# Optimization experiments

Hardware: AMD Instinct MI355X
Metric: run time of the kernel (lower is better)

## Reference

```python
import jax, jax.numpy as jnp
import numpy as np

NUM_GRAPHS = 256


def gcn_conv(x, W, b, src, dst, n_nodes):
    """PyG GCNConv: add self-loops, symmetric normalization, linear transform."""
    h = x @ W  # [N, out]
    loop = jnp.arange(n_nodes, dtype=src.dtype)
    src_f = jnp.concatenate([src, loop])  # messages j -> i, with self-loops
    dst_f = jnp.concatenate([dst, loop])
    deg = jax.ops.segment_sum(jnp.ones_like(src_f, dtype=h.dtype), dst_f,
                              num_segments=n_nodes)  # in-degree incl. self-loop
    dinv = jnp.where(deg > 0, jax.lax.rsqrt(deg), 0.0)
    norm = dinv[src_f] * dinv[dst_f]  # [E+N]
    msg = h[src_f] * norm[:, None]  # gather + scale, [E+N, out]
    out = jax.ops.segment_sum(msg, dst_f, num_segments=n_nodes)  # scatter-add
    return out + b


def global_mean_pool(x, batch, num_graphs):
    sums = jax.ops.segment_sum(x, batch, num_segments=num_graphs)
    cnt = jax.ops.segment_sum(jnp.ones((x.shape[0],), x.dtype), batch,
                              num_segments=num_graphs)
    return sums / jnp.maximum(cnt, 1.0)[:, None]


def setup_inputs() -> dict:
    key = jax.random.key(0)
    k = jax.random.split(key, 6)
    N, E, D = 50000, 800000, 133
    x = jax.random.normal(k[0], (N, D), dtype=jnp.float32)
    edge_index = jax.random.randint(k[1], (2, E), 0, N, dtype=jnp.int64)
    batch = jnp.sort(jax.random.randint(k[2], (N,), 0, NUM_GRAPHS, dtype=jnp.int64))
    s = 1.0 / np.sqrt(D)
    W1 = jax.random.normal(k[3], (D, D), dtype=jnp.float32) * s
    b1 = jnp.zeros((D,), jnp.float32)
    W2 = jax.random.normal(k[4], (D, D), dtype=jnp.float32) * s
    b2 = jnp.zeros((D,), jnp.float32)
    return {"x": x, "edge_index": edge_index, "batch": batch,
            "W1": W1, "b1": b1, "W2": W2, "b2": b2}


def reference(x, edge_index, batch, W1, b1, W2, b2):
    n = x.shape[0]
    src, dst = edge_index[0], edge_index[1]
    h = jax.nn.relu(gcn_conv(x, W1, b1, src, dst, n))
    h = jax.nn.relu(gcn_conv(h, W2, b2, src, dst, n))
    return global_mean_pool(h, batch, NUM_GRAPHS)  # [num_graphs, 133]
```

## Files before the change

kernel.cpp:

```cpp
#include <hip/hip_runtime.h>

#define D 133
#define DPB 160
#define NCGB 17
#define NGRAPH 256
#define KS 168
#define NT 9
#define CAP 64

typedef short short8 __attribute__((ext_vector_type(8)));
typedef float float4v __attribute__((ext_vector_type(4)));

__device__ __forceinline__ unsigned short f2bf(float x) {
    unsigned int u = __float_as_uint(x);
    u += 0x7fffu + ((u >> 16) & 1u);
    return (unsigned short)(u >> 16);
}

__device__ __forceinline__ void cvt8(uint4 v, float* f) {
    f[0] = __uint_as_float(v.x << 16);
    f[1] = __uint_as_float(v.x & 0xffff0000u);
    f[2] = __uint_as_float(v.y << 16);
    f[3] = __uint_as_float(v.y & 0xffff0000u);
    f[4] = __uint_as_float(v.z << 16);
    f[5] = __uint_as_float(v.z & 0xffff0000u);
    f[6] = __uint_as_float(v.w << 16);
    f[7] = __uint_as_float(v.w & 0xffff0000u);
}

__global__ __launch_bounds__(256) void k_wt(const float* __restrict__ W1,
                                            unsigned short* __restrict__ WT1,
                                            const float* __restrict__ W2,
                                            unsigned short* __restrict__ WT2,
                                            int wtB) {
    int bid = blockIdx.x;
    const float* W = (bid < wtB) ? W1 : W2;
    unsigned short* WT = (bid < wtB) ? WT1 : WT2;
    int lb = (bid < wtB) ? bid : bid - wtB;
    int i = lb * 256 + threadIdx.x;
    if (i < 144 * KS) {
        int n = i / KS, k = i - n * KS;
        WT[i] = (n < D && k < D) ? f2bf(W[(size_t)k * D + n]) : (unsigned short)0;
    }
}

__global__ __launch_bounds__(256, 2) void k_big(const float* __restrict__ X,
                                                const unsigned short* __restrict__ WTg,
                                                unsigned short* __restrict__ Y,
                                                const int* __restrict__ src,
                                                const int* __restrict__ dst,
                                                int* __restrict__ cnt,
                                                unsigned short* __restrict__ earr,
                                                const int* __restrict__ batch,
                                                int* __restrict__ gstart,
                                                int N, int E, int mt, int nib) {
    int bid = blockIdx.x, t = threadIdx.x;
    if (bid < nib) {
        int g = bid / 5, pos = bid - g * 5;
        if (pos != 4) {
            int i = (g * 4 + pos) * 256 + t;
            if (i < E) {
                int s = src[i];
                int dnode = dst[i];
                int slot = atomicAdd(&cnt[dnode], 1);
                if (slot < CAP) earr[(size_t)dnode * CAP + slot] = (unsigned short)s;
            }
            return;
        }
        int wave = t >> 6, lane = t & 63;
        int ln16 = lane & 15, quad = lane >> 4;
        int tile = g * 4 + wave;
        if (tile >= mt) return;
        int row0 = tile * 16;
        int ra = row0 + ln16; if (ra > N - 1) ra = N - 1;
        const float* Xr = X + (size_t)ra * D;
        const unsigned short* Wr = WTg + (size_t)ln16 * KS + quad * 8;

        float4v acc[NT];
        #pragma unroll
        for (int n = 0; n < NT; ++n) acc[n] = {0.f, 0.f, 0.f, 0.f};

        #pragma unroll
        for (int kk = 0; kk < 5; ++kk) {
            int cbase = kk * 32 + quad * 8;
            short8 a;
            if (kk < 4) {
                #pragma unroll
                for (int j = 0; j < 8; ++j) a[j] = (short)f2bf(Xr[cbase + j]);
            } else {
                #pragma unroll
                for (int j = 0; j < 8; ++j) {
                    int c = cbase + j;
                    a[j] = (short)((c < D) ? f2bf(Xr[c]) : 0);
                }
            }
            #pragma unroll
            for (int n = 0; n < NT; ++n) {
                short8 b = *(const short8*)(Wr + n * 16 * KS + kk * 32);
                acc[n] = __builtin_amdgcn_mfma_f32_16x16x32_bf16(a, b, acc[n], 0, 0, 0);
            }
        }
        #pragma unroll
        for (int r = 0; r < 4; ++r) {
            int row = row0 + quad * 4 + r;
            if (row < N) {
                unsigned short* Yr = Y + (size_t)row * DPB + ln16;
                #pragma unroll
                for (int n = 0; n < NT; ++n) Yr[n * 16] = f2bf(acc[n][r]);
            }
        }
        return;
    }
    bid -= nib;
    {
        int g = bid * 256 + t;
        if (g > NGRAPH) return;
        int lo = 0, hi = N;
        while (lo < hi) {
            int mid = (lo + hi) >> 1;
            if (batch[mid] < g) lo = mid + 1; else hi = mid;
        }
        gstart[g] = lo;
    }
}

__global__ __launch_bounds__(256, 2) void k_mm2(const unsigned short* __restrict__ A,
                                                const unsigned short* __restrict__ WTg,
                                                unsigned short* __restrict__ Y,
                                                int N, int mt) {
    int t = threadIdx.x;
    int wave = t >> 6, lane = t & 63;
    int ln16 = lane & 15, quad = lane >> 4;
    int tile = blockIdx.x * 4 + wave;
    if (tile >= mt) return;
    int row0 = tile * 16;
    int ra = row0 + ln16; if (ra > N - 1) ra = N - 1;
    const unsigned short* Ar = A + (size_t)ra * DPB + quad * 8;
    const unsigned short* Wr = WTg + (size_t)ln16 * KS + quad * 8;

    float4v acc[NT];
    #pragma unroll
    for (int n = 0; n < NT; ++n) acc[n] = {0.f, 0.f, 0.f, 0.f};

    #pragma unroll
    for (int kk = 0; kk < 5; ++kk) {
        short8 a = *(const short8*)(Ar + kk * 32);
        #pragma unroll
        for (int n = 0; n < NT; ++n) {
            short8 b = *(const short8*)(Wr + n * 16 * KS + kk * 32);
            acc[n] = __builtin_amdgcn_mfma_f32_16x16x32_bf16(a, b, acc[n], 0, 0, 0);
        }
    }
    #pragma unroll
    for (int r = 0; r < 4; ++r) {
        int row = row0 + quad * 4 + r;
        if (row < N) {
            unsigned short* Yr = Y + (size_t)row * DPB + ln16;
            #pragma unroll
            for (int n = 0; n < NT; ++n) Yr[n * 16] = f2bf(acc[n][r]);
        }
    }
}

__global__ __launch_bounds__(256) void k_agg(const unsigned short* __restrict__ H,
                                             const float* __restrict__ bias,
                                             const int* __restrict__ cnt,
                                             const unsigned short* __restrict__ earr,
                                             unsigned short* __restrict__ outb, int N) {
    int idx = blockIdx.x * 256 + threadIdx.x;
    if (idx >= N * NCGB) return;
    int node = idx / NCGB;
    int cg = idx - node * NCGB;
    int c = cg << 3;
    int degraw = cnt[node];
    float di = rsqrtf((float)(degraw + 1));
    float acc[8], f[8];
    uint4 hv = *(const uint4*)(H + (size_t)node * DPB + c);
    cvt8(hv, f);
    #pragma unroll
    for (int j = 0; j < 8; ++j) acc[j] = di * f[j];
    int deg = degraw > CAP ? CAP : degraw;
    const unsigned short* ep = earr + (size_t)node * CAP;
    int e = 0;
    for (; e + 4 <= deg; e += 4) {
        int s0 = ep[e], s1 = ep[e+1], s2 = ep[e+2], s3 = ep[e+3];
        float w0 = rsqrtf((float)(cnt[s0] + 1));
        float w1 = rsqrtf((float)(cnt[s1] + 1));
        float w2 = rsqrtf((float)(cnt[s2] + 1));
        float w3 = rsqrtf((float)(cnt[s3] + 1));
        uint4 v0 = *(const uint4*)(H + (size_t)s0 * DPB + c);
        uint4 v1 = *(const uint4*)(H + (size_t)s1 * DPB + c);
        uint4 v2 = *(const uint4*)(H + (size_t)s2 * DPB + c);
        uint4 v3 = *(const uint4*)(H + (size_t)s3 * DPB + c);
        cvt8(v0, f);
        #pragma unroll
        for (int j = 0; j < 8; ++j) acc[j] = fmaf(w0, f[j], acc[j]);
        cvt8(v1, f);
        #pragma unroll
        for (int j = 0; j < 8; ++j) acc[j] = fmaf(w1, f[j], acc[j]);
        cvt8(v2, f);
        #pragma unroll
        for (int j = 0; j < 8; ++j) acc[j] = fmaf(w2, f[j], acc[j]);
        cvt8(v3, f);
        #pragma unroll
        for (int j = 0; j < 8; ++j) acc[j] = fmaf(w3, f[j], acc[j]);
    }
    for (; e < deg; ++e) {
        int s = ep[e];
        float wv = rsqrtf((float)(cnt[s] + 1));
        uint4 v = *(const uint4*)(H + (size_t)s * DPB + c);
        cvt8(v, f);
        #pragma unroll
        for (int j = 0; j < 8; ++j) acc[j] = fmaf(wv, f[j], acc[j]);
    }
    float b[8];
    #pragma unroll
    for (int j = 0; j < 8; ++j) b[j] = (c + j < D) ? bias[c + j] : 0.f;
    unsigned int p[4];
    #pragma unroll
    for (int j = 0; j < 4; ++j) {
        float lo = fmaxf(fmaf(di, acc[2*j],   b[2*j]),   0.f);
        float hi = fmaxf(fmaf(di, acc[2*j+1], b[2*j+1]), 0.f);
        p[j] = (unsigned int)f2bf(lo) | ((unsigned int)f2bf(hi) << 16);
    }
    uint4 pk = {p[0], p[1], p[2], p[3]};
    unsigned short* o = outb + (size_t)node * DPB + c;
    *(uint4*)o = pk;
    if (cg == 16) {
        uint4 z = {0u, 0u, 0u, 0u};
        *(uint4*)(o + 8)  = z;
        *(uint4*)(o + 16) = z;
        *(uint4*)(o + 24) = z;
    }
}

__global__ __launch_bounds__(256) void k_pool(const unsigned short* __restrict__ H,
                                              const int* __restrict__ gstart,
                                              float* __restrict__ out) {
    int g = blockIdx.x / NCGB;
    int cg = blockIdx.x - g * NCGB;
    int c = cg << 3;
    int t = threadIdx.x;
    int s = gstart[g], e = gstart[g + 1];
    float acc[8], f[8];
    #pragma unroll
    for (int j = 0; j < 8; ++j) acc[j] = 0.f;
    for (int i = s + t; i < e; i += 256) {
        uint4 v = *(const uint4*)(H + (size_t)i * DPB + c);
        cvt8(v, f);
        #pragma unroll
        for (int j = 0; j < 8; ++j) acc[j] += f[j];
    }
    #pragma unroll
    for (int off = 32; off >= 1; off >>= 1) {
        #pragma unroll
        for (int j = 0; j < 8; ++j) acc[j] += __shfl_down(acc[j], off, 64);
    }
    __shared__ float part[4][8];
    int wave = t >> 6, lane = t & 63;
    if (lane == 0) {
        #pragma unroll
        for (int j = 0; j < 8; ++j) part[wave][j] = acc[j];
    }
    __syncthreads();
    if (t < 8) {
        int col = c + t;
        if (col < D) {
            float v = part[0][t] + part[1][t] + part[2][t] + part[3][t];
            float n = (float)(e - s);
            out[(size_t)g * D + col] = v / fmaxf(n, 1.f);
        }
    }
}

extern "C" void kernel_launch(void* const* d_in, const int* in_sizes, int n_in,
                              void* d_out, int out_size, void* d_ws, size_t ws_size,
                              hipStream_t stream) {
    const float* x   = (const float*)d_in[0];
    const int* ei    = (const int*)d_in[1];
    const int* batch = (const int*)d_in[2];
    const float* W1  = (const float*)d_in[3];
    const float* b1  = (const float*)d_in[4];
    const float* W2  = (const float*)d_in[5];
    const float* b2  = (const float*)d_in[6];
    float* out = (float*)d_out;

    int N = in_sizes[0] / D;
    int E = in_sizes[1] / 2;
    const int* src = ei;
    const int* dst = ei + E;

    char* w = (char*)d_ws;
    unsigned short* HbA = (unsigned short*)w; w += (size_t)N * DPB * 2;
    unsigned short* HbB = (unsigned short*)w; w += (size_t)N * DPB * 2;
    int* cnt            = (int*)w;            w += (size_t)N * 4;
    unsigned short* earr= (unsigned short*)w; w += (size_t)N * CAP * 2;
    int* gstart         = (int*)w;            w += (size_t)(NGRAPH + 1) * 4;
    unsigned short* WT1 = (unsigned short*)w; w += (size_t)144 * KS * 2;
    unsigned short* WT2 = (unsigned short*)w; w += (size_t)144 * KS * 2;

    int wtB   = (144 * KS + 255) / 256;
    int gsB   = (NGRAPH + 1 + 255) / 256;

    int mt = (N + 15) / 16;
    int mmB = (mt + 3) / 4;
    int nib = 5 * mmB;
    int grid_agg = (N * NCGB + 255) / 256;

    hipMemsetAsync(cnt, 0, (size_t)N * 4, stream);
    k_wt  <<<2 * wtB, 256, 0, stream>>>(W1, WT1, W2, WT2, wtB);
    k_big <<<nib + gsB, 256, 0, stream>>>(x, WT1, HbA, src, dst, cnt, earr,
                                          batch, gstart, N, E, mt, nib);
    k_agg <<<grid_agg, 256, 0, stream>>>(HbA, b1, cnt, earr, HbB, N);
    k_mm2 <<<mmB, 256, 0, stream>>>(HbB, WT2, HbA, N, mt);
    k_agg <<<grid_agg, 256, 0, stream>>>(HbA, b2, cnt, earr, HbB, N);
    k_pool<<<NGRAPH * NCGB, 256, 0, stream>>>(HbB, gstart, out);
}
```

Baseline: 257.2 us.

## Fuse layer-1 aggregation with layer-2 GEMM and fold memset into prep kernel

```diff
diff --git a/kernel.cpp b/kernel.cpp
--- a/kernel.cpp
+++ b/kernel.cpp
@@ -5,6 +5,7 @@
 #define NCGB 17
 #define NGRAPH 256
 #define KS 168
+#define LSTR 168
 #define NT 9
 #define CAP 64
 
@@ -32,15 +33,38 @@
                                             unsigned short* __restrict__ WT1,
                                             const float* __restrict__ W2,
                                             unsigned short* __restrict__ WT2,
-                                            int wtB) {
-    int bid = blockIdx.x;
-    const float* W = (bid < wtB) ? W1 : W2;
-    unsigned short* WT = (bid < wtB) ? WT1 : WT2;
-    int lb = (bid < wtB) ? bid : bid - wtB;
-    int i = lb * 256 + threadIdx.x;
-    if (i < 144 * KS) {
-        int n = i / KS, k = i - n * KS;
-        WT[i] = (n < D && k < D) ? f2bf(W[(size_t)k * D + n]) : (unsigned short)0;
+                                            int* __restrict__ cnt,
+                                            const int* __restrict__ batch,
+                                            int* __restrict__ gstart,
+                                            int N, int wtB, int czB) {
+    int bid = blockIdx.x, t = threadIdx.x;
+    if (bid < 2 * wtB) {
+        const float* W = (bid < wtB) ? W1 : W2;
+        unsigned short* WT = (bid < wtB) ? WT1 : WT2;
+        int lb = (bid < wtB) ? bid : bid - wtB;
+        int i = lb * 256 + t;
+        if (i < 144 * KS) {
+            int n = i / KS, k = i - n * KS;
+            WT[i] = (n < D && k < D) ? f2bf(W[(size_t)k * D + n]) : (unsigned short)0;
+        }
+        return;
+    }
+    bid -= 2 * wtB;
+    if (bid < czB) {
+        int i = bid * 256 + t;
+        if (i < N) cnt[i] = 0;
+        return;
+    }
+    bid -= czB;
+    {
+        int g = bid * 256 + t;
+        if (g > NGRAPH) return;
+        int lo = 0, hi = N;
+        while (lo < hi) {
+            int mid = (lo + hi) >> 1;
+            if (batch[mid] < g) lo = mid + 1; else hi = mid;
+        }
+        gstart[g] = lo;
     }
 }
 
@@ -51,91 +75,26 @@
                                                 const int* __restrict__ dst,
                                                 int* __restrict__ cnt,
                                                 unsigned short* __restrict__ earr,
-                                                const int* __restrict__ batch,
-                                                int* __restrict__ gstart,
-                                                int N, int E, int mt, int nib) {
+                                                int N, int E, int mt) {
     int bid = blockIdx.x, t = threadIdx.x;
-    if (bid < nib) {
-        int g = bid / 5, pos = bid - g * 5;
-        if (pos != 4) {
-            int i = (g * 4 + pos) * 256 + t;
-            if (i < E) {
-                int s = src[i];
-                int dnode = dst[i];
-                int slot = atomicAdd(&cnt[dnode], 1);
-                if (slot < CAP) earr[(size_t)dnode * CAP + slot] = (unsigned short)s;
-            }
-            return;
-        }
-        int wave = t >> 6, lane = t & 63;
-        int ln16 = lane & 15, quad = lane >> 4;
-        int tile = g * 4 + wave;
-        if (tile >= mt) return;
-        int row0 = tile * 16;
-        int ra = row0 + ln16; if (ra > N - 1) ra = N - 1;
-        const float* Xr = X + (size_t)ra * D;
-        const unsigned short* Wr = WTg + (size_t)ln16 * KS + quad * 8;
-
-        float4v acc[NT];
-        #pragma unroll
-        for (int n = 0; n < NT; ++n) acc[n] = {0.f, 0.f, 0.f, 0.f};
-
-        #pragma unroll
-        for (int kk = 0; kk < 5; ++kk) {
-            int cbase = kk * 32 + quad * 8;
-            short8 a;
-            if (kk < 4) {
-                #pragma unroll
-                for (int j = 0; j < 8; ++j) a[j] = (short)f2bf(Xr[cbase + j]);
-            } else {
-                #pragma unroll
-                for (int j = 0; j < 8; ++j) {
-                    int c = cbase + j;
-                    a[j] = (short)((c < D) ? f2bf(Xr[c]) : 0);
-                }
-            }
-            #pragma unroll
-            for (int n = 0; n < NT; ++n) {
-                short8 b = *(const short8*)(Wr + n * 16 * KS + kk * 32);
-                acc[n] = __builtin_amdgcn_mfma_f32_16x16x32_bf16(a, b, acc[n], 0, 0, 0);
-            }
-        }
-        #pragma unroll
-        for (int r = 0; r < 4; ++r) {
-            int row = row0 + quad * 4 + r;
-            if (row < N) {
-                unsigned short* Yr = Y + (size_t)row * DPB + ln16;
-                #pragma unroll
-                for (int n = 0; n < NT; ++n) Yr[n * 16] = f2bf(acc[n][r]);
-            }
+    int g = bid / 5, pos = bid - g * 5;
+    if (pos != 4) {
+        int i = (g * 4 + pos) * 256 + t;
+        if (i < E) {
+            int s = src[i];
+            int dnode = dst[i];
+            int slot = atomicAdd(&cnt[dnode], 1);
+            if (slot < CAP) earr[(size_t)dnode * CAP + slot] = (unsigned short)s;
         }
         return;
     }
-    bid -= nib;
-    {
-        int g = bid * 256 + t;
-        if (g > NGRAPH) return;
-        int lo = 0, hi = N;
-        while (lo < hi) {
-            int mid = (lo + hi) >> 1;
-            if (batch[mid] < g) lo = mid + 1; else hi = mid;
-        }
-        gstart[g] = lo;
-    }
-}
-
-__global__ __launch_bounds__(256, 2) void k_mm2(const unsigned short* __restrict__ A,
-                                                const unsigned short* __restrict__ WTg,
-                                                unsigned short* __restrict__ Y,
-                                                int N, int mt) {
-    int t = threadIdx.x;
     int wave = t >> 6, lane = t & 63;
     int ln16 = lane & 15, quad = lane >> 4;
-    int tile = blockIdx.x * 4 + wave;
+    int tile = g * 4 + wave;
     if (tile >= mt) return;
     int row0 = tile * 16;
     int ra = row0 + ln16; if (ra > N - 1) ra = N - 1;
-    const unsigned short* Ar = A + (size_t)ra * DPB + quad * 8;
+    const float* Xr = X + (size_t)ra * D;
     const unsigned short* Wr = WTg + (size_t)ln16 * KS + quad * 8;
 
     float4v acc[NT];
@@ -144,7 +103,18 @@
 
     #pragma unroll
     for (int kk = 0; kk < 5; ++kk) {
-        short8 a = *(const short8*)(Ar + kk * 32);
+        int cbase = kk * 32 + quad * 8;
+        short8 a;
+        if (kk < 4) {
+            #pragma unroll
+            for (int j = 0; j < 8; ++j) a[j] = (short)f2bf(Xr[cbase + j]);
+        } else {
+            #pragma unroll
+            for (int j = 0; j < 8; ++j) {
+                int c = cbase + j;
+                a[j] = (short)((c < D) ? f2bf(Xr[c]) : 0);
+            }
+        }
         #pragma unroll
         for (int n = 0; n < NT; ++n) {
             short8 b = *(const short8*)(Wr + n * 16 * KS + kk * 32);
@@ -162,11 +132,107 @@
     }
 }
 
-__global__ __launch_bounds__(256) void k_agg(const unsigned short* __restrict__ H,
-                                             const float* __restrict__ bias,
-                                             const int* __restrict__ cnt,
-                                             const unsigned short* __restrict__ earr,
-                                             unsigned short* __restrict__ outb, int N) {
+__global__ __launch_bounds__(320, 2) void k_aggmm(const unsigned short* __restrict__ H,
+                                                  const float* __restrict__ bias,
+                                                  const int* __restrict__ cnt,
+                                                  const unsigned short* __restrict__ earr,
+                                                  const unsigned short* __restrict__ WTg,
+                                                  unsigned short* __restrict__ Y, int N) {
+    __shared__ unsigned short T[16 * LSTR];
+    int t = threadIdx.x;
+    int row0 = blockIdx.x * 16;
+    if (t < 272) {
+        int l = t / NCGB;
+        int cg = t - l * NCGB;
+        int node = row0 + l;
+        if (node >= N) node = N - 1;
+        int c = cg << 3;
+        int degraw = cnt[node];
+        float di = rsqrtf((float)(degraw + 1));
+        float acc[8], f[8];
+        uint4 hv = *(const uint4*)(H + (size_t)node * DPB + c);
+        cvt8(hv, f);
+        #pragma unroll
+        for (int j = 0; j < 8; ++j) acc[j] = di * f[j];
+        int deg = degraw > CAP ? CAP : degraw;
+        const unsigned short* ep = earr + (size_t)node * CAP;
+        int e = 0;
+        for (; e + 4 <= deg; e += 4) {
+            int s0 = ep[e], s1 = ep[e+1], s2 = ep[e+2], s3 = ep[e+3];
+            float w0 = rsqrtf((float)(cnt[s0] + 1));
+            float w1 = rsqrtf((float)(cnt[s1] + 1));
+            float w2 = rsqrtf((float)(cnt[s2] + 1));
+            float w3 = rsqrtf((float)(cnt[s3] + 1));
+            uint4 v0 = *(const uint4*)(H + (size_t)s0 * DPB + c);
+            uint4 v1 = *(const uint4*)(H + (size_t)s1 * DPB + c);
+            uint4 v2 = *(const uint4*)(H + (size_t)s2 * DPB + c);
+            uint4 v3 = *(const uint4*)(H + (size_t)s3 * DPB + c);
+            cvt8(v0, f);
+            #pragma unroll
+            for (int j = 0; j < 8; ++j) acc[j] = fmaf(w0, f[j], acc[j]);
+            cvt8(v1, f);
+            #pragma unroll
+            for (int j = 0; j < 8; ++j) acc[j] = fmaf(w1, f[j], acc[j]);
+            cvt8(v2, f);
+            #pragma unroll
+            for (int j = 0; j < 8; ++j) acc[j] = fmaf(w2, f[j], acc[j]);
+            cvt8(v3, f);
+            #pragma unroll
+            for (int j = 0; j < 8; ++j) acc[j] = fmaf(w3, f[j], acc[j]);
+        }
+        for (; e < deg; ++e) {
+            int s = ep[e];
+            float wv = rsqrtf((float)(cnt[s] + 1));
+            uint4 v = *(const uint4*)(H + (size_t)s * DPB + c);
+            cvt8(v, f);
+            #pragma unroll
+            for (int j = 0; j < 8; ++j) acc[j] = fmaf(wv, f[j], acc[j]);
+        }
+        float b[8];
+        #pragma unroll
+        for (int j = 0; j < 8; ++j) b[j] = (c + j < D) ? bias[c + j] : 0.f;
+        unsigned int p[4];
+        #pragma unroll
+        for (int j = 0; j < 4; ++j) {
+            float lo = fmaxf(fmaf(di, acc[2*j],   b[2*j]),   0.f);
+            float hi = fmaxf(fmaf(di, acc[2*j+1], b[2*j+1]), 0.f);
+            p[j] = (unsigned int)f2bf(lo) | ((unsigned int)f2bf(hi) << 16);
+        }
+        uint4 pk = {p[0], p[1], p[2], p[3]};
+        *(uint4*)(T + l * LSTR + c) = pk;
+    } else {
+        int k = t - 272;
+        int l = k / 3, seg = k - l * 3;
+        uint4 z = {0u, 0u, 0u, 0u};
+        *(uint4*)(T + l * LSTR + 136 + seg * 8) = z;
+    }
+    __syncthreads();
+
+    int wave = t >> 6, lane = t & 63;
+    int ln16 = lane & 15, quad = lane >> 4;
+    const unsigned short* Ar = T + ln16 * LSTR + quad * 8;
+    const unsigned short* Wr = WTg + (size_t)ln16 * KS + quad * 8;
+    for (int n = wave; n < NT; n += 5) {
+        float4v acc2 = {0.f, 0.f, 0.f, 0.f};
+        #pragma unroll
+        for (int kk = 0; kk < 5; ++kk) {
+            short8 a = *(const short8*)(Ar + kk * 32);
+            short8 b = *(const short8*)(Wr + n * 16 * KS + kk * 32);
+            acc2 = __builtin_amdgcn_mfma_f32_16x16x32_bf16(a, b, acc2, 0, 0, 0);
+        }
+        #pragma unroll
+        for (int r = 0; r < 4; ++r) {
+            int row = row0 + quad * 4 + r;
+            if (row < N) Y[(size_t)row * DPB + n * 16 + ln16] = f2bf(acc2[r]);
+        }
+    }
+}
+
+__global__ __launch_bounds__(256) void k_agg2(const unsigned short* __restrict__ H,
+                                              const float* __restrict__ bias,
+                                              const int* __restrict__ cnt,
+                                              const unsigned short* __restrict__ earr,
+                                              unsigned short* __restrict__ outb, int N) {
     int idx = blockIdx.x * 256 + threadIdx.x;
     if (idx >= N * NCGB) return;
     int node = idx / NCGB;
@@ -224,14 +290,7 @@
         p[j] = (unsigned int)f2bf(lo) | ((unsigned int)f2bf(hi) << 16);
     }
     uint4 pk = {p[0], p[1], p[2], p[3]};
-    unsigned short* o = outb + (size_t)node * DPB + c;
-    *(uint4*)o = pk;
-    if (cg == 16) {
-        uint4 z = {0u, 0u, 0u, 0u};
-        *(uint4*)(o + 8)  = z;
-        *(uint4*)(o + 16) = z;
-        *(uint4*)(o + 24) = z;
-    }
+    *(uint4*)(outb + (size_t)node * DPB + c) = pk;
 }
 
 __global__ __launch_bounds__(256) void k_pool(const unsigned short* __restrict__ H,
@@ -299,20 +358,19 @@
     unsigned short* WT1 = (unsigned short*)w; w += (size_t)144 * KS * 2;
     unsigned short* WT2 = (unsigned short*)w; w += (size_t)144 * KS * 2;
 
-    int wtB   = (144 * KS + 255) / 256;
-    int gsB   = (NGRAPH + 1 + 255) / 256;
+    int wtB = (144 * KS + 255) / 256;
+    int czB = (N + 255) / 256;
+    int gsB = (NGRAPH + 1 + 255) / 256;
 
     int mt = (N + 15) / 16;
     int mmB = (mt + 3) / 4;
     int nib = 5 * mmB;
     int grid_agg = (N * NCGB + 255) / 256;
 
-    hipMemsetAsync(cnt, 0, (size_t)N * 4, stream);
-    k_wt  <<<2 * wtB, 256, 0, stream>>>(W1, WT1, W2, WT2, wtB);
-    k_big <<<nib + gsB, 256, 0, stream>>>(x, WT1, HbA, src, dst, cnt, earr,
-                                          batch, gstart, N, E, mt, nib);
-    k_agg <<<grid_agg, 256, 0, stream>>>(HbA, b1, cnt, earr, HbB, N);
-    k_mm2 <<<mmB, 256, 0, stream>>>(HbB, WT2, HbA, N, mt);
-    k_agg <<<grid_agg, 256, 0, stream>>>(HbA, b2, cnt, earr, HbB, N);
-    k_pool<<<NGRAPH * NCGB, 256, 0, stream>>>(HbB, gstart, out);
-}
+    k_wt    <<<2 * wtB + czB + gsB, 256, 0, stream>>>(W1, WT1, W2, WT2, cnt,
+                                                      batch, gstart, N, wtB, czB);
+    k_big   <<<nib, 256, 0, stream>>>(x, WT1, HbA, src, dst, cnt, earr, N, E, mt);
+    k_aggmm <<<mt, 320, 0, stream>>>(HbA, b1, cnt, earr, WT2, HbB, N);
+    k_agg2  <<<grid_agg, 256, 0, stream>>>(HbB, b2, cnt, earr, HbA, N);
+    k_pool  <<<NGRAPH * NCGB, 256, 0, stream>>>(HbA, gstart, out);
+}
```

After: 249.5 us. -3.0%, faster.

## Store GEMM outputs in column-blocked layout and aggregate per column block

Applied to the files above, without the earlier changes.

```diff
diff --git a/kernel.cpp b/kernel.cpp
--- a/kernel.cpp
+++ b/kernel.cpp
@@ -1,12 +1,13 @@
 #include <hip/hip_runtime.h>
 
 #define D 133
-#define DPB 160
+#define DPB 136
 #define NCGB 17
 #define NGRAPH 256
 #define KS 168
 #define NT 9
 #define CAP 64
+#define NPB 85
 
 typedef short short8 __attribute__((ext_vector_type(8)));
 typedef float float4v __attribute__((ext_vector_type(4)));
@@ -28,19 +29,43 @@
     f[7] = __uint_as_float(v.w & 0xffff0000u);
 }
 
+
 __global__ __launch_bounds__(256) void k_wt(const float* __restrict__ W1,
                                             unsigned short* __restrict__ WT1,
                                             const float* __restrict__ W2,
                                             unsigned short* __restrict__ WT2,
-                                            int wtB) {
-    int bid = blockIdx.x;
-    const float* W = (bid < wtB) ? W1 : W2;
-    unsigned short* WT = (bid < wtB) ? WT1 : WT2;
-    int lb = (bid < wtB) ? bid : bid - wtB;
-    int i = lb * 256 + threadIdx.x;
-    if (i < 144 * KS) {
-        int n = i / KS, k = i - n * KS;
-        WT[i] = (n < D && k < D) ? f2bf(W[(size_t)k * D + n]) : (unsigned short)0;
+                                            int* __restrict__ cnt,
+                                            const int* __restrict__ batch,
+                                            int* __restrict__ gstart,
+                                            int N, int wtB, int czB) {
+    int bid = blockIdx.x, t = threadIdx.x;
+    if (bid < 2 * wtB) {
+        const float* W = (bid < wtB) ? W1 : W2;
+        unsigned short* WT = (bid < wtB) ? WT1 : WT2;
+        int lb = (bid < wtB) ? bid : bid - wtB;
+        int i = lb * 256 + t;
+        if (i < 144 * KS) {
+            int n = i / KS, k = i - n * KS;
+            WT[i] = (n < D && k < D) ? f2bf(W[(size_t)k * D + n]) : (unsigned short)0;
+        }
+        return;
+    }
+    bid -= 2 * wtB;
+    if (bid < czB) {
+        int i = bid * 256 + t;
+        if (i < N) cnt[i] = 0;
+        return;
+    }
+    bid -= czB;
+    {
+        int g = bid * 256 + t;
+        if (g > NGRAPH) return;
+        int lo = 0, hi = N;
+        while (lo < hi) {
+            int mid = (lo + hi) >> 1;
+            if (batch[mid] < g) lo = mid + 1; else hi = mid;
+        }
+        gstart[g] = lo;
     }
 }
 
@@ -51,77 +76,138 @@
                                                 const int* __restrict__ dst,
                                                 int* __restrict__ cnt,
                                                 unsigned short* __restrict__ earr,
-                                                const int* __restrict__ batch,
-                                                int* __restrict__ gstart,
-                                                int N, int E, int mt, int nib) {
+                                                int N, int E, int mt) {
     int bid = blockIdx.x, t = threadIdx.x;
-    if (bid < nib) {
-        int g = bid / 5, pos = bid - g * 5;
-        if (pos != 4) {
-            int i = (g * 4 + pos) * 256 + t;
-            if (i < E) {
-                int s = src[i];
-                int dnode = dst[i];
-                int slot = atomicAdd(&cnt[dnode], 1);
-                if (slot < CAP) earr[(size_t)dnode * CAP + slot] = (unsigned short)s;
+    int g = bid / 5, pos = bid - g * 5;
+    if (pos != 4) {
+        int i = (g * 4 + pos) * 256 + t;
+        if (i < E) {
+            int s = src[i];
+            int dnode = dst[i];
+            int slot = atomicAdd(&cnt[dnode], 1);
+            if (slot < CAP) earr[(size_t)dnode * CAP + slot] = (unsigned short)s;
+        }
+        return;
+    }
+    int wave = t >> 6, lane = t & 63;
+    int ln16 = lane & 15, quad = lane >> 4;
+    int tile = g * 4 + wave;
+    if (tile >= mt) return;
+    int row0 = tile * 16;
+    int ra = row0 + ln16; if (ra > N - 1) ra = N - 1;
+    const float* Xr = X + (size_t)ra * D;
+    const unsigned short* Wr = WTg + (size_t)ln16 * KS + quad * 8;
+
+    float4v acc[NT];
+    #pragma unroll
+    for (int n = 0; n < NT; ++n) acc[n] = {0.f, 0.f, 0.f, 0.f};
+
+    #pragma unroll
+    for (int kk = 0; kk < 5; ++kk) {
+        int cbase = kk * 32 + quad * 8;
+        short8 a;
+        if (kk < 4) {
+            #pragma unroll
+            for (int j = 0; j < 8; ++j) a[j] = (short)f2bf(Xr[cbase + j]);
+        } else {
+            #pragma unroll
+            for (int j = 0; j < 8; ++j) {
+                int c = cbase + j;
+                a[j] = (short)((c < D) ? f2bf(Xr[c]) : 0);
             }
-            return;
-        }
-        int wave = t >> 6, lane = t & 63;
-        int ln16 = lane & 15, quad = lane >> 4;
-        int tile = g * 4 + wave;
-        if (tile >= mt) return;
-        int row0 = tile * 16;
-        int ra = row0 + ln16; if (ra > N - 1) ra = N - 1;
-        const float* Xr = X + (size_t)ra * D;
-        const unsigned short* Wr = WTg + (size_t)ln16 * KS + quad * 8;
-
-        float4v acc[NT];
-        #pragma unroll
-        for (int n = 0; n < NT; ++n) acc[n] = {0.f, 0.f, 0.f, 0.f};
-
-        #pragma unroll
-        for (int kk = 0; kk < 5; ++kk) {
-            int cbase = kk * 32 + quad * 8;
-            short8 a;
-            if (kk < 4) {
-                #pragma unroll
-                for (int j = 0; j < 8; ++j) a[j] = (short)f2bf(Xr[cbase + j]);
-            } else {
-                #pragma unroll
-                for (int j = 0; j < 8; ++j) {
-                    int c = cbase + j;
-                    a[j] = (short)((c < D) ? f2bf(Xr[c]) : 0);
-                }
-            }
+        }
+        #pragma unroll
+        for (int n = 0; n < NT; ++n) {
+            short8 b = *(const short8*)(Wr + n * 16 * KS + kk * 32);
+            acc[n] = __builtin_amdgcn_mfma_f32_16x16x32_bf16(a, b, acc[n], 0, 0, 0);
+        }
+    }
+    #pragma unroll
+    for (int r = 0; r < 4; ++r) {
+        int row = row0 + quad * 4 + r;
+        if (row < N) {
             #pragma unroll
-            for (int n = 0; n < NT; ++n) {
-                short8 b = *(const short8*)(Wr + n * 16 * KS + kk * 32);
-                acc[n] = __builtin_amdgcn_mfma_f32_16x16x32_bf16(a, b, acc[n], 0, 0, 0);
-            }
-        }
-        #pragma unroll
-        for (int r = 0; r < 4; ++r) {
-            int row = row0 + quad * 4 + r;
-            if (row < N) {
-                unsigned short* Yr = Y + (size_t)row * DPB + ln16;
-                #pragma unroll
-                for (int n = 0; n < NT; ++n) Yr[n * 16] = f2bf(acc[n][r]);
-            }
-        }
-        return;
-    }
-    bid -= nib;
-    {
-        int g = bid * 256 + t;
-        if (g > NGRAPH) return;
-        int lo = 0, hi = N;
-        while (lo < hi) {
-            int mid = (lo + hi) >> 1;
-            if (batch[mid] < g) lo = mid + 1; else hi = mid;
-        }
-        gstart[g] = lo;
-    }
+            for (int n = 0; n < 7; ++n)
+                Y[((size_t)n * N + row) * 16 + ln16] = f2bf(acc[n][r]);
+            unsigned short* y7 = Y + (size_t)7 * N * 16 + (size_t)row * 24;
+            y7[ln16] = f2bf(acc[7][r]);
+            if (ln16 < 8) y7[16 + ln16] = f2bf(acc[8][r]);
+        }
+    }
+}
+
+__global__ __launch_bounds__(256) void k_aggcb(const unsigned short* __restrict__ H,
+                                               const float* __restrict__ bias,
+                                               const int* __restrict__ cnt,
+                                               const unsigned short* __restrict__ earr,
+                                               unsigned short* __restrict__ outb, int N) {
+    int cb = blockIdx.x & 7;
+    int chunk = blockIdx.x >> 3;
+    int tpn = (cb == 7) ? 3 : 2;
+    int t = threadIdx.x;
+    int local = t / tpn;
+    int sub = t - local * tpn;
+    if (local >= NPB) return;
+    int node = chunk * NPB + local;
+    if (node >= N) return;
+    int cg = (cb < 7) ? cb * 2 + sub : 14 + sub;
+    size_t st = (cb < 7) ? 16 : 24;
+    const unsigned short* Hb = (cb < 7) ? H + (size_t)cb * N * 16 + sub * 8
+                                        : H + (size_t)7 * N * 16 + sub * 8;
+    int degraw = cnt[node];
+    float di = rsqrtf((float)(degraw + 1));
+    float acc[8], f[8];
+    uint4 hv = *(const uint4*)(Hb + (size_t)node * st);
+    cvt8(hv, f);
+    #pragma unroll
+    for (int j = 0; j < 8; ++j) acc[j] = di * f[j];
+    int deg = degraw > CAP ? CAP : degraw;
+    const unsigned short* ep = earr + (size_t)node * CAP;
+    int e = 0;
+    for (; e + 4 <= deg; e += 4) {
+        int s0 = ep[e], s1 = ep[e+1], s2 = ep[e+2], s3 = ep[e+3];
+        float w0 = rsqrtf((float)(cnt[s0] + 1));
+        float w1 = rsqrtf((float)(cnt[s1] + 1));
+        float w2 = rsqrtf((float)(cnt[s2] + 1));
+        float w3 = rsqrtf((float)(cnt[s3] + 1));
+        uint4 v0 = *(const uint4*)(Hb + (size_t)s0 * st);
+        uint4 v1 = *(const uint4*)(Hb + (size_t)s1 * st);
+        uint4 v2 = *(const uint4*)(Hb + (size_t)s2 * st);
+        uint4 v3 = *(const uint4*)(Hb + (size_t)s3 * st);
+        cvt8(v0, f);
+        #pragma unroll
+        for (int j = 0; j < 8; ++j) acc[j] = fmaf(w0, f[j], acc[j]);
+        cvt8(v1, f);
+        #pragma unroll
+        for (int j = 0; j < 8; ++j) acc[j] = fmaf(w1, f[j], acc[j]);
+        cvt8(v2, f);
+        #pragma unroll
+        for (int j = 0; j < 8; ++j) acc[j] = fmaf(w2, f[j], acc[j]);
+        cvt8(v3, f);
+        #pragma unroll
+        for (int j = 0; j < 8; ++j) acc[j] = fmaf(w3, f[j], acc[j]);
+    }
+    for (; e < deg; ++e) {
+        int s = ep[e];
+        float wv = rsqrtf((float)(cnt[s] + 1));
+        uint4 v = *(const uint4*)(Hb + (size_t)s * st);
+        cvt8(v, f);
+        #pragma unroll
+        for (int j = 0; j < 8; ++j) acc[j] = fmaf(wv, f[j], acc[j]);
+    }
+    int c0 = cg << 3;
+    float b[8];
+    #pragma unroll
+    for (int j = 0; j < 8; ++j) b[j] = (c0 + j < D) ? bias[c0 + j] : 0.f;
+    unsigned int p[4];
+    #pragma unroll
+    for (int j = 0; j < 4; ++j) {
+        float lo = fmaxf(fmaf(di, acc[2*j],   b[2*j]),   0.f);
+        float hi = fmaxf(fmaf(di, acc[2*j+1], b[2*j+1]), 0.f);
+        p[j] = (unsigned int)f2bf(lo) | ((unsigned int)f2bf(hi) << 16);
+    }
+    uint4 pk = {p[0], p[1], p[2], p[3]};
+    *(uint4*)(outb + (size_t)node * DPB + c0) = pk;
 }
 
 __global__ __launch_bounds__(256, 2) void k_mm2(const unsigned short* __restrict__ A,
@@ -144,7 +230,14 @@
 
     #pragma unroll
     for (int kk = 0; kk < 5; ++kk) {
-        short8 a = *(const short8*)(Ar + kk * 32);
+        short8 a;
+        if (kk < 4) {
+            a = *(const short8*)(Ar + kk * 32);
+        } else if (quad == 0) {
+            a = *(const short8*)(A + (size_t)ra * DPB + 128);
+        } else {
+            a = (short8){0, 0, 0, 0, 0, 0, 0, 0};
+        }
         #pragma unroll
         for (int n = 0; n < NT; ++n) {
             short8 b = *(const short8*)(Wr + n * 16 * KS + kk * 32);
@@ -155,82 +248,13 @@
     for (int r = 0; r < 4; ++r) {
         int row = row0 + quad * 4 + r;
         if (row < N) {
-            unsigned short* Yr = Y + (size_t)row * DPB + ln16;
             #pragma unroll
-            for (int n = 0; n < NT; ++n) Yr[n * 16] = f2bf(acc[n][r]);
-        }
-    }
-}
-
-__global__ __launch_bounds__(256) void k_agg(const unsigned short* __restrict__ H,
-                                             const float* __restrict__ bias,
-                                             const int* __restrict__ cnt,
-                                             const unsigned short* __restrict__ earr,
-                                             unsigned short* __restrict__ outb, int N) {
-    int idx = blockIdx.x * 256 + threadIdx.x;
-    if (idx >= N * NCGB) return;
-    int node = idx / NCGB;
-    int cg = idx - node * NCGB;
-    int c = cg << 3;
-    int degraw = cnt[node];
-    float di = rsqrtf((float)(degraw + 1));
-    float acc[8], f[8];
-    uint4 hv = *(const uint4*)(H + (size_t)node * DPB + c);
-    cvt8(hv, f);
-    #pragma unroll
-    for (int j = 0; j < 8; ++j) acc[j] = di * f[j];
-    int deg = degraw > CAP ? CAP : degraw;
-    const unsigned short* ep = earr + (size_t)node * CAP;
-    int e = 0;
-    for (; e + 4 <= deg; e += 4) {
-        int s0 = ep[e], s1 = ep[e+1], s2 = ep[e+2], s3 = ep[e+3];
-        float w0 = rsqrtf((float)(cnt[s0] + 1));
-        float w1 = rsqrtf((float)(cnt[s1] + 1));
-        float w2 = rsqrtf((float)(cnt[s2] + 1));
-        float w3 = rsqrtf((float)(cnt[s3] + 1));
-        uint4 v0 = *(const uint4*)(H + (size_t)s0 * DPB + c);
-        uint4 v1 = *(const uint4*)(H + (size_t)s1 * DPB + c);
-        uint4 v2 = *(const uint4*)(H + (size_t)s2 * DPB + c);
-        uint4 v3 = *(const uint4*)(H + (size_t)s3 * DPB + c);
-        cvt8(v0, f);
-        #pragma unroll
-        for (int j = 0; j < 8; ++j) acc[j] = fmaf(w0, f[j], acc[j]);
-        cvt8(v1, f);
-        #pragma unroll
-        for (int j = 0; j < 8; ++j) acc[j] = fmaf(w1, f[j], acc[j]);
-        cvt8(v2, f);
-        #pragma unroll
-        for (int j = 0; j < 8; ++j) acc[j] = fmaf(w2, f[j], acc[j]);
-        cvt8(v3, f);
-        #pragma unroll
-        for (int j = 0; j < 8; ++j) acc[j] = fmaf(w3, f[j], acc[j]);
-    }
-    for (; e < deg; ++e) {
-        int s = ep[e];
-        float wv = rsqrtf((float)(cnt[s] + 1));
-        uint4 v = *(const uint4*)(H + (size_t)s * DPB + c);
-        cvt8(v, f);
-        #pragma unroll
-        for (int j = 0; j < 8; ++j) acc[j] = fmaf(wv, f[j], acc[j]);
-    }
-    float b[8];
-    #pragma unroll
-    for (int j = 0; j < 8; ++j) b[j] = (c + j < D) ? bias[c + j] : 0.f;
-    unsigned int p[4];
-    #pragma unroll
-    for (int j = 0; j < 4; ++j) {
-        float lo = fmaxf(fmaf(di, acc[2*j],   b[2*j]),   0.f);
-        float hi = fmaxf(fmaf(di, acc[2*j+1], b[2*j+1]), 0.f);
-        p[j] = (unsigned int)f2bf(lo) | ((unsigned int)f2bf(hi) << 16);
-    }
-    uint4 pk = {p[0], p[1], p[2], p[3]};
-    unsigned short* o = outb + (size_t)node * DPB + c;
-    *(uint4*)o = pk;
-    if (cg == 16) {
-        uint4 z = {0u, 0u, 0u, 0u};
-        *(uint4*)(o + 8)  = z;
-        *(uint4*)(o + 16) = z;
-        *(uint4*)(o + 24) = z;
+            for (int n = 0; n < 7; ++n)
+                Y[((size_t)n * N + row) * 16 + ln16] = f2bf(acc[n][r]);
+            unsigned short* y7 = Y + (size_t)7 * N * 16 + (size_t)row * 24;
+            y7[ln16] = f2bf(acc[7][r]);
+            if (ln16 < 8) y7[16 + ln16] = f2bf(acc[8][r]);
+        }
     }
 }
 
@@ -291,28 +315,29 @@
     const int* dst = ei + E;
 
     char* w = (char*)d_ws;
-    unsigned short* HbA = (unsigned short*)w; w += (size_t)N * DPB * 2;
-    unsigned short* HbB = (unsigned short*)w; w += (size_t)N * DPB * 2;
+    unsigned short* HbA = (unsigned short*)w; w += ((size_t)N * DPB + 64) * 2;
+    unsigned short* HbB = (unsigned short*)w; w += ((size_t)N * DPB + 64) * 2;
     int* cnt            = (int*)w;            w += (size_t)N * 4;
     unsigned short* earr= (unsigned short*)w; w += (size_t)N * CAP * 2;
     int* gstart         = (int*)w;            w += (size_t)(NGRAPH + 1) * 4;
     unsigned short* WT1 = (unsigned short*)w; w += (size_t)144 * KS * 2;
     unsigned short* WT2 = (unsigned short*)w; w += (size_t)144 * KS * 2;
 
-    int wtB   = (144 * KS + 255) / 256;
-    int gsB   = (NGRAPH + 1 + 255) / 256;
+    int wtB = (144 * KS + 255) / 256;
+    int czB = (N + 255) / 256;
+    int gsB = (NGRAPH + 1 + 255) / 256;
 
     int mt = (N + 15) / 16;
     int mmB = (mt + 3) / 4;
     int nib = 5 * mmB;
-    int grid_agg = (N * NCGB + 255) / 256;
-
-    hipMemsetAsync(cnt, 0, (size_t)N * 4, stream);
-    k_wt  <<<2 * wtB, 256, 0, stream>>>(W1, WT1, W2, WT2, wtB);
-    k_big <<<nib + gsB, 256, 0, stream>>>(x, WT1, HbA, src, dst, cnt, earr,
-                                          batch, gstart, N, E, mt, nib);
-    k_agg <<<grid_agg, 256, 0, stream>>>(HbA, b1, cnt, earr, HbB, N);
-    k_mm2 <<<mmB, 256, 0, stream>>>(HbB, WT2, HbA, N, mt);
-    k_agg <<<grid_agg, 256, 0, stream>>>(HbA, b2, cnt, earr, HbB, N);
-    k_pool<<<NGRAPH * NCGB, 256, 0, stream>>>(HbB, gstart, out);
-}
+    int chunks = (N + NPB - 1) / NPB;
+    int grid_agg = chunks * 8;
+
+    k_wt    <<<2 * wtB + czB + gsB, 256, 0, stream>>>(W1, WT1, W2, WT2, cnt,
+                                                      batch, gstart, N, wtB, czB);
+    k_big   <<<nib, 256, 0, stream>>>(x, WT1, HbA, src, dst, cnt, earr, N, E, mt);
+    k_aggcb <<<grid_agg, 256, 0, stream>>>(HbA, b1, cnt, earr, HbB, N);
+    k_mm2   <<<mmB, 256, 0, stream>>>(HbB, WT2, HbA, N, mt);
+    k_aggcb <<<grid_agg, 256, 0, stream>>>(HbA, b2, cnt, earr, HbB, N);
+    k_pool  <<<NGRAPH * NCGB, 256, 0, stream>>>(HbB, gstart, out);
+}
```

Result: slower. 334.2 us (+30.0%).
